# Kernel tuning notes

Measured on AMD Instinct MI355X. Metric: run time of the kernel, lower is better.

Reference implementation:

```python
import jax, jax.numpy as jnp
import numpy as np

N = 8192      # total nodes
BG = 8        # graphs in batch
NPG = 1024    # nodes per graph
DEG = 8       # in-degree per node
E = N * DEG   # edges
Q = 16        # queries per graph
D = 768       # in_dim
H = 4         # heads
F = 768       # h_feats per head
HD = H * F    # 3072


def setup_inputs() -> dict:
    key = jax.random.key(0)
    ks = jax.random.split(key, 24)
    x = jax.random.normal(ks[0], (N, D), jnp.float32)
    # block-diagonal random graph: every node has DEG incoming edges from its own graph
    edge_dst = jnp.repeat(jnp.arange(N), DEG)
    edge_src = (edge_dst // NPG) * NPG + jax.random.randint(ks[1], (E,), 0, NPG)
    query_embedding = jax.random.normal(ks[2], (BG, Q, D), jnp.float32) * 0.02
    bert_score = jax.random.uniform(ks[3], (BG, Q, NPG), jnp.float32)

    def lin(k, i, o):
        return jax.random.normal(k, (i, o), jnp.float32) * (1.0 / np.sqrt(i))

    inp = dict(x=x, edge_src=edge_src, edge_dst=edge_dst,
               query_embedding=query_embedding, bert_score=bert_score)
    inp['W1'] = lin(ks[4], D, HD)
    inp['attn_l1'] = jax.random.normal(ks[5], (H, F), jnp.float32) * 0.1
    inp['attn_r1'] = jax.random.normal(ks[6], (H, F), jnp.float32) * 0.1
    inp['b1'] = jax.random.normal(ks[7], (HD,), jnp.float32) * 0.02
    inp['gamma1'] = 1.0 + 0.1 * jax.random.normal(ks[8], (HD,), jnp.float32)
    inp['beta1'] = 0.1 * jax.random.normal(ks[9], (HD,), jnp.float32)
    inp['prelu1'] = 0.25 + 0.01 * jax.random.normal(ks[10], (HD,), jnp.float32)
    inp['W2'] = lin(ks[11], HD, HD)
    inp['attn_l2'] = jax.random.normal(ks[12], (H, F), jnp.float32) * 0.1
    inp['attn_r2'] = jax.random.normal(ks[13], (H, F), jnp.float32) * 0.1
    inp['b2'] = jax.random.normal(ks[14], (HD,), jnp.float32) * 0.02
    inp['gamma2'] = 1.0 + 0.1 * jax.random.normal(ks[15], (HD,), jnp.float32)
    inp['beta2'] = 0.1 * jax.random.normal(ks[16], (HD,), jnp.float32)
    inp['prelu2'] = 0.25 + 0.01 * jax.random.normal(ks[17], (HD,), jnp.float32)
    return inp


def _gat_layer(h, src, dst, W, al, ar, b, gamma, beta, pa):
    # DGL GATConv (eval mode, no residual): fc -> edge attention -> segment softmax -> scatter-sum
    feat = (h @ W).reshape(N, H, F)
    el = jnp.einsum('nhf,hf->nh', feat, al)            # [N,H]
    er = jnp.einsum('nhf,hf->nh', feat, ar)
    e = el[src] + er[dst]                              # [E,H]
    e = jnp.where(e > 0, e, 0.2 * e)                   # leaky_relu(0.2)
    m = jax.ops.segment_max(e, dst, num_segments=N)
    a = jnp.exp(e - m[dst])
    denom = jax.ops.segment_sum(a, dst, num_segments=N)
    alpha = a / denom[dst]                             # edge softmax over in-edges
    rst = jax.ops.segment_sum(feat[src] * alpha[:, :, None], dst, num_segments=N)
    hflat = (rst + b.reshape(1, H, F)).reshape(N, HD)
    # BatchNorm1d (training-mode batch statistics, biased var)
    mu = hflat.mean(axis=0)
    var = hflat.var(axis=0)
    hn = (hflat - mu) * jax.lax.rsqrt(var + 1e-5) * gamma + beta
    # PReLU (per-channel)
    return jnp.where(hn > 0, hn, pa * hn)


def _lambda_mrr(y_pred, y_true):
    # y_pred/y_true: [Q,K]; no padding in this pipeline (y_true = 1/rank > 0)
    order = jnp.argsort(-y_pred, axis=-1)
    yp = jnp.take_along_axis(y_pred, order, axis=-1)
    yt = jnp.take_along_axis(y_true, order, axis=-1)
    mask = (yt[:, :, None] - yt[:, None, :] > 0).astype(yp.dtype)
    sdiff = jnp.clip(yp[:, :, None] - yp[:, None, :], -50.0, 50.0)
    losses = jnp.log1p(jnp.exp(-sdiff))
    return (losses * mask).sum() / mask.sum()


def _forward(x, edge_src, edge_dst, query_embedding, bert_score,
             W1, attn_l1, attn_r1, b1, gamma1, beta1, prelu1,
             W2, attn_l2, attn_r2, b2, gamma2, beta2, prelu2):
    h1 = _gat_layer(x, edge_src, edge_dst, W1, attn_l1, attn_r1, b1, gamma1, beta1, prelu1)
    m1 = h1.reshape(N, H, F).mean(axis=1)
    h2 = _gat_layer(h1, edge_src, edge_dst, W2, attn_l2, attn_r2, b2, gamma2, beta2, prelu2)
    m2 = h2.reshape(N, H, F).mean(axis=1)
    node_rep = jnp.maximum(m1, m2)                      # JumpingKnowledge(max)

    reps = node_rep.reshape(BG, NPG, F)                 # per-graph reps
    reps_flat = node_rep                                # [N,F]
    graph_of = jnp.repeat(jnp.arange(BG), NPG)          # [N]
    rank_gt = (1.0 / jnp.arange(1, NPG + 1, dtype=jnp.float32))[None, :]  # [1,K]

    def per_graph(i, rep_i, q, bs):
        order = jnp.argsort(-bs, axis=-1)               # [Q,NPG] bert rank (desc)
        p = rep_i[order[:, 0]]                          # [Q,F] positive
        neg = rep_i[order[:, 1:]]                       # [Q,NPG-1,F] own negatives
        p_sim = jnp.sum(q * p, axis=-1, keepdims=True)  # [Q,1]
        own_sim = jnp.einsum('qf,qkf->qk', q, neg)      # [Q,NPG-1]
        all_sim = q @ reps_flat.T                       # [Q,N] for in-batch negatives
        other = (graph_of != i).astype(q.dtype)         # mask out own graph
        rank_pred = jnp.concatenate([p_sim, own_sim], axis=-1)  # first K cols of ranking_list
        mrr = _lambda_mrr(rank_pred, jnp.broadcast_to(rank_gt, rank_pred.shape))
        pe = jnp.exp(p_sim).sum(axis=-1)
        ne = jnp.exp(own_sim).sum(axis=-1) + (jnp.exp(all_sim) * other).sum(axis=-1)
        cl = jnp.mean(-jnp.log(pe / (pe + ne)))
        logp = jax.nn.log_softmax(q @ rep_i.T, axis=-1)
        ent = jnp.mean(-(jnp.exp(logp) * logp).sum(axis=-1))
        return cl, mrr, ent

    cl_g, mrr_g, ent_g = jax.vmap(per_graph)(jnp.arange(BG), reps, query_embedding, bert_score)
    return cl_g.mean(), mrr_g.mean(), ent_g.mean()


def reference(x, edge_src, edge_dst, query_embedding, bert_score,
              W1, attn_l1, attn_r1, b1, gamma1, beta1, prelu1,
              W2, attn_l2, attn_r2, b2, gamma2, beta2, prelu2):
    return _forward(x, edge_src, edge_dst, query_embedding, bert_score,
                    W1, attn_l1, attn_r1, b1, gamma1, beta1, prelu1,
                    W2, attn_l2, attn_r2, b2, gamma2, beta2, prelu2)
```

## Files before the change

kernel.cpp:

```cpp
#include <hip/hip_runtime.h>
#include <hip/hip_bf16.h>
#include <hip/hip_fp16.h>

#define NN 8192
#define DD 768
#define HH 4
#define FF 768
#define HD 3072
#define BGr 8
#define NPGr 1024
#define QQ 16
#define NQ 128
#define DEGr 8
#define MRR_TILES 36
#define WSCALE 32.0f
#define WSCALE_INV 0.03125f

typedef __attribute__((ext_vector_type(8))) short bf16x8;
typedef __attribute__((ext_vector_type(4))) float f32x4;
typedef __attribute__((ext_vector_type(4))) int i32x4;
typedef __attribute__((ext_vector_type(8))) int i32x8;

__device__ __forceinline__ unsigned short f2bf(float f) {
    union { float f; unsigned u; } v; v.f = f;
    unsigned u = v.u;
    unsigned r = (u + 0x7fffu + ((u >> 16) & 1u)) >> 16;
    return (unsigned short)r;
}
__device__ __forceinline__ float bf2f(unsigned short u) {
    union { unsigned u; float f; } v; v.u = ((unsigned)u) << 16;
    return v.f;
}
__device__ __forceinline__ unsigned char f2fp8(float x) {
    unsigned s = (__float_as_uint(x) >> 24) & 0x80;
    __half h = __float2half(fabsf(x) * 0.00390625f);
    unsigned t = (unsigned)__half_as_ushort(h);
    t += 0x3F + ((t >> 7) & 1);
    unsigned b = t >> 7;
    if (b > 0x7E) b = 0x7E;
    return (unsigned char)(s | b);
}
__device__ __forceinline__ float fp82f(unsigned u) {
    unsigned short hb = (unsigned short)(((u & 0x80) << 8) | ((u & 0x7F) << 7));
    return __half2float(__ushort_as_half(hb)) * 256.f;
}

__device__ __forceinline__ void gl_lds16(const void* g, void* l) {
    __builtin_amdgcn_global_load_lds(
        (const __attribute__((address_space(1))) unsigned int*)g,
        (__attribute__((address_space(3))) unsigned int*)l, 16, 0, 0);
}

#define PB_Z 13
#define PB_CX (PB_Z + 6144)
#define PB_CQ (PB_CX + 96)
#define PB_T1 (PB_CQ + 2304)
#define PB_T2 (PB_T1 + 9216)
__global__ __launch_bounds__(256) void prep_k(const float* __restrict__ x,
                                              unsigned char* __restrict__ xb,
                                              const float* __restrict__ qe,
                                              unsigned short* __restrict__ qeb,
                                              const float* __restrict__ W1,
                                              unsigned char* __restrict__ w1t,
                                              const float* __restrict__ W2,
                                              unsigned char* __restrict__ w2t,
                                              float* __restrict__ stats1,
                                              float* __restrict__ stats2,
                                              float* __restrict__ out) {
    __shared__ float tile[32][33];
    int blk = blockIdx.x, tid = threadIdx.x;
    if (blk < PB_Z) {
        int f = blk * 1024 + tid * 4;
        if (f < 2 * HD) *(float4*)&stats1[f] = make_float4(0.f, 0.f, 0.f, 0.f);
        else if (f < 4 * HD) *(float4*)&stats2[f - 2 * HD] = make_float4(0.f, 0.f, 0.f, 0.f);
        else if (f == 4 * HD) { out[0] = 0.f; out[1] = 0.f; out[2] = 0.f; }
    } else if (blk < PB_CX) {
        int i = (blk - PB_Z) * 256 + tid;
        float4 v = ((const float4*)x)[i];
        uchar4 o;
        o.x = f2fp8(v.x); o.y = f2fp8(v.y); o.z = f2fp8(v.z); o.w = f2fp8(v.w);
        ((uchar4*)xb)[i] = o;
    } else if (blk < PB_CQ) {
        int i = (blk - PB_CX) * 256 + tid;
        float4 v = ((const float4*)qe)[i];
        ushort4 o;
        o.x = f2bf(v.x); o.y = f2bf(v.y); o.z = f2bf(v.z); o.w = f2bf(v.w);
        ((ushort4*)qeb)[i] = o;
    } else {
        const float* in; unsigned char* outp; int K, t;
        if (blk < PB_T1) { in = W1; outp = w1t; K = DD; t = blk - PB_CQ; }
        else             { in = W2; outp = w2t; K = HD; t = blk - PB_T1; }
        int n0 = (t % 96) * 32, k0 = (t / 96) * 32;
        int tx = tid & 31, ty = tid >> 5;
        #pragma unroll
        for (int i = 0; i < 4; i++) {
            int r = ty + i * 8;
            tile[r][tx] = in[(size_t)(k0 + r) * HD + n0 + tx];
        }
        __syncthreads();
        #pragma unroll
        for (int i = 0; i < 4; i++) {
            int r = ty + i * 8;
            outp[(size_t)(n0 + r) * K + k0 + tx] = f2fp8(tile[tx][r] * WSCALE);
        }
    }
}

template <bool EPI>
__global__ __launch_bounds__(256) void gemm_fp8(const unsigned char* __restrict__ A,
                                                const unsigned char* __restrict__ BT,
                                                unsigned char* __restrict__ C,
                                                float* __restrict__ elp,
                                                float* __restrict__ erp,
                                                const float* __restrict__ al,
                                                const float* __restrict__ ar,
                                                int M, int Nc, int K, float inv_scale) {
    __shared__ __align__(16) unsigned char As[128 * 128];
    __shared__ __align__(16) unsigned char Bs[128 * 128];
    int tid = threadIdx.x;
    int m0 = blockIdx.x * 128;
    int n0 = blockIdx.y * 128;
    int w = tid >> 6, lane = tid & 63;
    int wr = w >> 1, wc = w & 1;
    int lm = lane & 15, lq = lane >> 4;

    f32x4 acc[4][4] = {};

    int srow = tid >> 3, su = tid & 7;
    const unsigned char* Ag[4];
    const unsigned char* Bg[4];
    unsigned char* AsW[4];
    unsigned char* BsW[4];
    #pragma unroll
    for (int s = 0; s < 4; s++) {
        int row = srow + 32 * s;
        int uu = su ^ (row & 7);
        Ag[s]  = A  + (size_t)(m0 + row) * K + uu * 16;
        Bg[s]  = BT + (size_t)(n0 + row) * K + uu * 16;
        AsW[s] = &As[row * 128 + su * 16];
        BsW[s] = &Bs[row * 128 + su * 16];
    }

    for (int k0 = 0; k0 < K; k0 += 128) {
        __syncthreads();
        #pragma unroll
        for (int s = 0; s < 4; s++) {
            gl_lds16(Ag[s], AsW[s]);
            gl_lds16(Bg[s], BsW[s]);
        }
        __syncthreads();

        i32x8 af[4];
        #pragma unroll
        for (int i = 0; i < 4; i++) {
            int row = wr * 64 + i * 16 + lm;
            int sw = (row & 7) << 4;
            i32x4 lo = *(const i32x4*)&As[row * 128 + ((lq * 32) ^ sw)];
            i32x4 hi = *(const i32x4*)&As[row * 128 + ((lq * 32 + 16) ^ sw)];
            i32x8 v;
            v[0] = lo[0]; v[1] = lo[1]; v[2] = lo[2]; v[3] = lo[3];
            v[4] = hi[0]; v[5] = hi[1]; v[6] = hi[2]; v[7] = hi[3];
            af[i] = v;
        }
        #pragma unroll
        for (int j = 0; j < 4; j++) {
            int row = wc * 64 + j * 16 + lm;
            int sw = (row & 7) << 4;
            i32x4 lo = *(const i32x4*)&Bs[row * 128 + ((lq * 32) ^ sw)];
            i32x4 hi = *(const i32x4*)&Bs[row * 128 + ((lq * 32 + 16) ^ sw)];
            i32x8 bv;
            bv[0] = lo[0]; bv[1] = lo[1]; bv[2] = lo[2]; bv[3] = lo[3];
            bv[4] = hi[0]; bv[5] = hi[1]; bv[6] = hi[2]; bv[7] = hi[3];
            #pragma unroll
            for (int i = 0; i < 4; i++)
                acc[i][j] = __builtin_amdgcn_mfma_scale_f32_16x16x128_f8f6f4(
                    af[i], bv, acc[i][j], 0, 0, 0, 127, 0, 127);
        }

        #pragma unroll
        for (int s = 0; s < 4; s++) { Ag[s] += 128; Bg[s] += 128; }
    }

    #pragma unroll
    for (int i = 0; i < 4; i++)
        #pragma unroll
        for (int j = 0; j < 4; j++)
            #pragma unroll
            for (int r = 0; r < 4; r++)
                acc[i][j][r] *= inv_scale;

    #pragma unroll
    for (int i = 0; i < 4; i++) {
        int row = m0 + wr * 64 + i * 16 + lq * 4;
        #pragma unroll
        for (int j = 0; j < 4; j++) {
            int col = n0 + wc * 64 + j * 16 + lm;
            #pragma unroll
            for (int r = 0; r < 4; r++)
                C[(size_t)(row + r) * Nc + col] = f2fp8(acc[i][j][r]);
        }
    }

    if (EPI) {
        int h = n0 / FF;
        int cb = (n0 % FF) >> 7;
        float alv[4], arv[4];
        #pragma unroll
        for (int j = 0; j < 4; j++) {
            int col = n0 + wc * 64 + j * 16 + lm;
            alv[j] = al[col];
            arv[j] = ar[col];
        }
        #pragma unroll
        for (int i = 0; i < 4; i++) {
            #pragma unroll
            for (int r = 0; r < 4; r++) {
                float se = acc[i][0][r] * alv[0] + acc[i][1][r] * alv[1]
                         + acc[i][2][r] * alv[2] + acc[i][3][r] * alv[3];
                float sr_ = acc[i][0][r] * arv[0] + acc[i][1][r] * arv[1]
                          + acc[i][2][r] * arv[2] + acc[i][3][r] * arv[3];
                #pragma unroll
                for (int mm = 1; mm <= 8; mm <<= 1) {
                    se  += __shfl_xor(se, mm, 64);
                    sr_ += __shfl_xor(sr_, mm, 64);
                }
                if (lm == 0) {
                    int row = m0 + wr * 64 + i * 16 + lq * 4 + r;
                    size_t slot = ((size_t)row * HH + h) * 12 + cb * 2 + wc;
                    elp[slot] = se;
                    erp[slot] = sr_;
                }
            }
        }
    }
}

__global__ __launch_bounds__(256) void gemm_bt(const unsigned short* __restrict__ A,
                                               const unsigned short* __restrict__ BT,
                                               float* __restrict__ Ct,
                                               int M, int Nc, int K) {
    __shared__ unsigned short As[128 * 64];
    __shared__ unsigned short Bs[128 * 64];
    int tid = threadIdx.x;
    int m0 = blockIdx.x * 128;
    int n0 = blockIdx.y * 128;
    int w = tid >> 6, lane = tid & 63;
    int wr = w >> 1, wc = w & 1;
    int lm = lane & 15, lq = lane >> 4;

    f32x4 acc[4][4] = {};

    int pc = tid & 7;
    const unsigned short* Ag[4];
    const unsigned short* Bg[4];
    unsigned short* AsW[4];
    unsigned short* BsW[4];
    #pragma unroll
    for (int s = 0; s < 4; s++) {
        int row = (tid >> 3) + 32 * s;
        int lc = pc ^ (row & 7);
        Ag[s]  = A  + (size_t)(m0 + row) * K + lc * 8;
        Bg[s]  = BT + (size_t)(n0 + row) * K + lc * 8;
        AsW[s] = &As[(row * 8 + pc) * 8];
        BsW[s] = &Bs[(row * 8 + pc) * 8];
    }

    for (int k0 = 0; k0 < K; k0 += 64) {
        __syncthreads();
        #pragma unroll
        for (int s = 0; s < 4; s++) {
            gl_lds16(Ag[s], AsW[s]);
            gl_lds16(Bg[s], BsW[s]);
        }
        __syncthreads();

        #pragma unroll
        for (int kk = 0; kk < 2; kk++) {
            bf16x8 af[4], bfr[4];
            #pragma unroll
            for (int i = 0; i < 4; i++) {
                int row = wr * 64 + i * 16 + lm;
                int phys = (kk * 4 + lq) ^ (row & 7);
                af[i] = *(const bf16x8*)&As[row * 64 + phys * 8];
            }
            #pragma unroll
            for (int j = 0; j < 4; j++) {
                int row = wc * 64 + j * 16 + lm;
                int phys = (kk * 4 + lq) ^ (row & 7);
                bfr[j] = *(const bf16x8*)&Bs[row * 64 + phys * 8];
            }
            #pragma unroll
            for (int i = 0; i < 4; i++)
                #pragma unroll
                for (int j = 0; j < 4; j++)
                    acc[i][j] = __builtin_amdgcn_mfma_f32_16x16x32_bf16(af[i], bfr[j], acc[i][j], 0, 0, 0);
        }

        #pragma unroll
        for (int s = 0; s < 4; s++) { Ag[s] += 64; Bg[s] += 64; }
    }

    #pragma unroll
    for (int i = 0; i < 4; i++) {
        int row = m0 + wr * 64 + i * 16 + lq * 4;
        #pragma unroll
        for (int j = 0; j < 4; j++) {
            int col = n0 + wc * 64 + j * 16 + lm;
            float4 o = make_float4(acc[i][j][0], acc[i][j][1], acc[i][j][2], acc[i][j][3]);
            *(float4*)&Ct[(size_t)col * M + row] = o;
        }
    }
}

__global__ __launch_bounds__(384) void aggregate_k(const unsigned char* __restrict__ feat,
                                                   const float* __restrict__ elp,
                                                   const float* __restrict__ erp,
                                                   const int* __restrict__ esrc,
                                                   const float* __restrict__ bias,
                                                   unsigned short* __restrict__ out) {
    int b = blockIdx.x;
    int nbase = (b & 7) * NPGr + (b >> 3) * 8;
    int t = threadIdx.x;
    __shared__ int s_src[8][DEGr];
    __shared__ float s_el[8][DEGr][HH];
    __shared__ float s_er[8][HH];
    __shared__ float s_alpha[8][DEGr][HH];
    if (t < 64) s_src[t >> 3][t & 7] = esrc[(size_t)(nbase + (t >> 3)) * DEGr + (t & 7)];
    __syncthreads();
    if (t < 256) {
        int nd = t >> 5, k = (t >> 2) & 7, h = t & 3;
        const float* pp = &elp[((size_t)s_src[nd][k] * HH + h) * 12];
        float s = 0.f;
        #pragma unroll
        for (int q = 0; q < 12; q++) s += pp[q];
        s_el[nd][k][h] = s;
    }
    if (t < 32) {
        int nd = t >> 2, h = t & 3;
        const float* pp = &erp[((size_t)(nbase + nd) * HH + h) * 12];
        float s = 0.f;
        #pragma unroll
        for (int q = 0; q < 12; q++) s += pp[q];
        s_er[nd][h] = s;
    }
    __syncthreads();
    if (t < 32) {
        int nd = t >> 2, h = t & 3;
        float e[DEGr], m = -1e30f;
        #pragma unroll
        for (int k = 0; k < DEGr; k++) {
            float v = s_el[nd][k][h] + s_er[nd][h];
            v = v > 0.f ? v : 0.2f * v;
            e[k] = v; m = fmaxf(m, v);
        }
        float d = 0.f;
        #pragma unroll
        for (int k = 0; k < DEGr; k++) { e[k] = __expf(e[k] - m); d += e[k]; }
        float inv = 1.0f / d;
        #pragma unroll
        for (int k = 0; k < DEGr; k++) s_alpha[nd][k][h] = e[k] * inv;
    }
    __syncthreads();

    int c8 = t * 8;
    int h = t / 96;
    float4 b0 = *(const float4*)&bias[c8];
    float4 b1 = *(const float4*)&bias[c8 + 4];
    float bb[8] = {b0.x, b0.y, b0.z, b0.w, b1.x, b1.y, b1.z, b1.w};
    #pragma unroll
    for (int nd = 0; nd < 8; nd++) {
        float a[8] = {bb[0], bb[1], bb[2], bb[3], bb[4], bb[5], bb[6], bb[7]};
        #pragma unroll
        for (int k = 0; k < DEGr; k++) {
            float wv = s_alpha[nd][k][h];
            unsigned long fv = *(const unsigned long*)&feat[(size_t)s_src[nd][k] * HD + c8];
            #pragma unroll
            for (int e = 0; e < 8; e++)
                a[e] += wv * fp82f((unsigned)((fv >> (8 * e)) & 0xFF));
        }
        union { unsigned short u[8]; bf16x8 v; } o;
        #pragma unroll
        for (int e = 0; e < 8; e++) o.u[e] = f2bf(a[e]);
        *(bf16x8*)&out[(size_t)(nbase + nd) * HD + c8] = o.v;
    }
}

__global__ __launch_bounds__(256) void ln_stats_k(const unsigned short* __restrict__ x,
                                                  float* __restrict__ sums) {
    int col = (blockIdx.x * 256 + threadIdx.x) * 4;
    int r0 = blockIdx.y * 128;
    float s[4] = {0.f, 0.f, 0.f, 0.f}, s2[4] = {0.f, 0.f, 0.f, 0.f};
    for (int r = r0; r < r0 + 128; r++) {
        ushort4 v = *(const ushort4*)&x[(size_t)r * HD + col];
        float f0 = bf2f(v.x), f1 = bf2f(v.y), f2 = bf2f(v.z), f3 = bf2f(v.w);
        s[0] += f0; s[1] += f1; s[2] += f2; s[3] += f3;
        s2[0] += f0 * f0; s2[1] += f1 * f1; s2[2] += f2 * f2; s2[3] += f3 * f3;
    }
    #pragma unroll
    for (int e = 0; e < 4; e++) {
        atomicAdd(&sums[col + e], s[e]);
        atomicAdd(&sums[HD + col + e], s2[e]);
    }
}

__device__ __forceinline__ void ln_vals(const unsigned short* __restrict__ x, int n, int col,
                                        const float* __restrict__ sums,
                                        const float* __restrict__ gamma,
                                        const float* __restrict__ beta,
                                        const float* __restrict__ prelu,
                                        float* val) {
    const float invN = 1.0f / (float)NN;
    ushort4 v = *(const ushort4*)&x[(size_t)n * HD + col];
    float4 sm = *(const float4*)&sums[col];
    float4 sq = *(const float4*)&sums[HD + col];
    float4 g = *(const float4*)&gamma[col];
    float4 b = *(const float4*)&beta[col];
    float4 p = *(const float4*)&prelu[col];
    float vv[4] = {bf2f(v.x), bf2f(v.y), bf2f(v.z), bf2f(v.w)};
    float ss[4] = {sm.x, sm.y, sm.z, sm.w};
    float qq[4] = {sq.x, sq.y, sq.z, sq.w};
    float gg[4] = {g.x, g.y, g.z, g.w};
    float bb[4] = {b.x, b.y, b.z, b.w};
    float pp[4] = {p.x, p.y, p.z, p.w};
    #pragma unroll
    for (int e = 0; e < 4; e++) {
        float mu = ss[e] * invN;
        float var = qq[e] * invN - mu * mu;
        float rs = rsqrtf(var + 1e-5f);
        float t = (vv[e] - mu) * rs * gg[e] + bb[e];
        val[e] = t > 0.f ? t : pp[e] * t;
    }
}

__global__ __launch_bounds__(192) void ln_norm_mean_k(const unsigned short* __restrict__ x,
                                                      const float* __restrict__ sums,
                                                      const float* __restrict__ gamma,
                                                      const float* __restrict__ beta,
                                                      const float* __restrict__ prelu,
                                                      unsigned char* __restrict__ h,
                                                      unsigned short* __restrict__ m1) {
    int n = blockIdx.x, tid = threadIdx.x;
    int c = tid * 4;
    float acc4[4] = {0.f, 0.f, 0.f, 0.f};
    #pragma unroll
    for (int hh = 0; hh < HH; hh++) {
        int col = hh * FF + c;
        float val[4];
        ln_vals(x, n, col, sums, gamma, beta, prelu, val);
        uchar4 o;
        o.x = f2fp8(val[0]); o.y = f2fp8(val[1]); o.z = f2fp8(val[2]); o.w = f2fp8(val[3]);
        *(uchar4*)&h[(size_t)n * HD + col] = o;
        #pragma unroll
        for (int e = 0; e < 4; e++) acc4[e] += val[e];
    }
    ushort4 o;
    o.x = f2bf(0.25f * acc4[0]); o.y = f2bf(0.25f * acc4[1]);
    o.z = f2bf(0.25f * acc4[2]); o.w = f2bf(0.25f * acc4[3]);
    *(ushort4*)&m1[(size_t)n * FF + c] = o;
}

__global__ __launch_bounds__(192) void ln_norm_rep_k(const unsigned short* __restrict__ x,
                                                     const float* __restrict__ sums,
                                                     const float* __restrict__ gamma,
                                                     const float* __restrict__ beta,
                                                     const float* __restrict__ prelu,
                                                     const unsigned short* __restrict__ m1,
                                                     unsigned short* __restrict__ rep) {
    int n = blockIdx.x, tid = threadIdx.x;
    int c = tid * 4;
    float acc4[4] = {0.f, 0.f, 0.f, 0.f};
    #pragma unroll
    for (int hh = 0; hh < HH; hh++) {
        int col = hh * FF + c;
        float val[4];
        ln_vals(x, n, col, sums, gamma, beta, prelu, val);
        #pragma unroll
        for (int e = 0; e < 4; e++) acc4[e] += val[e];
    }
    ushort4 m = *(const ushort4*)&m1[(size_t)n * FF + c];
    ushort4 o;
    o.x = f2bf(fmaxf(bf2f(m.x), 0.25f * acc4[0]));
    o.y = f2bf(fmaxf(bf2f(m.y), 0.25f * acc4[1]));
    o.z = f2bf(fmaxf(bf2f(m.z), 0.25f * acc4[2]));
    o.w = f2bf(fmaxf(bf2f(m.w), 0.25f * acc4[3]));
    *(ushort4*)&rep[(size_t)n * FF + c] = o;
}

__global__ __launch_bounds__(256) void loss_k(const float* __restrict__ simsQ,
                                              const float* __restrict__ bert,
                                              float* __restrict__ out) {
    __shared__ float s_ya[128];
    __shared__ float s_ba[128];
    __shared__ float red[256];
    __shared__ int redi[256];
    int tid = threadIdx.x;

    if (blockIdx.x < NQ * MRR_TILES) {
        int qq = blockIdx.x / MRR_TILES;
        int t36 = blockIdx.x % MRR_TILES;
        int I = 0, rem = t36;
        while (rem >= 8 - I) { rem -= 8 - I; I++; }
        int J = I + rem;
        int g = qq >> 4;
        const float* Y = simsQ + (size_t)qq * NN + (size_t)g * NPGr;
        const float* B = bert + (size_t)qq * NPGr;
        int a0 = I * 128, b0 = J * 128;

        if (tid < 128) s_ya[tid] = Y[a0 + tid];
        else           s_ba[tid - 128] = B[a0 + (tid - 128)];
        int bl = tid & 127;
        int bcol = b0 + bl;
        float yb = Y[bcol];
        float bbv = B[bcol];
        __syncthreads();

        const float L2E = 1.44269504f;
        int abase = (tid >> 7) * 64;
        float s = 0.f;
        if (I == J) {
            #pragma unroll 4
            for (int ai = 0; ai < 64; ai++) {
                int a = abase + ai;
                float ya = s_ya[a], ba = s_ba[a];
                float tdf = ya - yb;
                float d = (bbv > ba) ? tdf : -tdf;
                float xv = fminf(fmaxf(d, -50.f), 50.f);
                float term = __builtin_amdgcn_logf(1.0f + __builtin_amdgcn_exp2f(xv * L2E));
                s += (bl > a) ? term : 0.f;
            }
        } else {
            #pragma unroll 4
            for (int ai = 0; ai < 64; ai++) {
                int a = abase + ai;
                float ya = s_ya[a], ba = s_ba[a];
                float tdf = ya - yb;
                float d = (bbv > ba) ? tdf : -tdf;
                float xv = fminf(fmaxf(d, -50.f), 50.f);
                s += __builtin_amdgcn_logf(1.0f + __builtin_amdgcn_exp2f(xv * L2E));
            }
        }
        red[tid] = s; __syncthreads();
        for (int o = 128; o; o >>= 1) { if (tid < o) red[tid] += red[tid + o]; __syncthreads(); }
        if (tid == 0)
            atomicAdd(&out[1], red[0] * (0.69314718f / (523776.0f * (float)NQ)));
    } else {
        int qq = blockIdx.x - NQ * MRR_TILES;
        int g = qq >> 4;
        const float* S = simsQ + (size_t)qq * NN;
        const float* Sg = S + g * NPGr;
        float m = -1e30f;
        for (int n = tid; n < NN; n += 256) m = fmaxf(m, S[n]);
        red[tid] = m; __syncthreads();
        for (int o = 128; o; o >>= 1) { if (tid < o) red[tid] = fmaxf(red[tid], red[tid + o]); __syncthreads(); }
        float mAll = red[0]; __syncthreads();
        float mg = -1e30f;
        for (int j = tid; j < NPGr; j += 256) mg = fmaxf(mg, Sg[j]);
        red[tid] = mg; __syncthreads();
        for (int o = 128; o; o >>= 1) { if (tid < o) red[tid] = fmaxf(red[tid], red[tid + o]); __syncthreads(); }
        float mG = red[0]; __syncthreads();
        float z = 0.f;
        for (int n = tid; n < NN; n += 256) z += __expf(S[n] - mAll);
        red[tid] = z; __syncthreads();
        for (int o = 128; o; o >>= 1) { if (tid < o) red[tid] += red[tid + o]; __syncthreads(); }
        float Zall = red[0]; __syncthreads();
        float zg = 0.f, tg = 0.f;
        for (int j = tid; j < NPGr; j += 256) {
            float s = Sg[j];
            float e = __expf(s - mG);
            zg += e; tg += e * s;
        }
        red[tid] = zg; __syncthreads();
        for (int o = 128; o; o >>= 1) { if (tid < o) red[tid] += red[tid + o]; __syncthreads(); }
        float Zg = red[0]; __syncthreads();
        red[tid] = tg; __syncthreads();
        for (int o = 128; o; o >>= 1) { if (tid < o) red[tid] += red[tid + o]; __syncthreads(); }
        float Tg = red[0]; __syncthreads();
        float bb = -1e30f; int bi = NPGr;
        for (int j = tid; j < NPGr; j += 256) {
            float v = bert[(size_t)qq * NPGr + j];
            if (v > bb) { bb = v; bi = j; }
        }
        red[tid] = bb; redi[tid] = bi; __syncthreads();
        for (int o = 128; o; o >>= 1) {
            if (tid < o) {
                if (red[tid + o] > red[tid] || (red[tid + o] == red[tid] && redi[tid + o] < redi[tid])) {
                    red[tid] = red[tid + o]; redi[tid] = redi[tid + o];
                }
            }
            __syncthreads();
        }
        if (tid == 0) {
            float p_sim = Sg[redi[0]];
            float lse = mAll + logf(Zall);
            atomicAdd(&out[0], (lse - p_sim) * (1.0f / (float)NQ));
            float entv = (mG + logf(Zg)) - Tg / Zg;
            atomicAdd(&out[2], entv * (1.0f / (float)NQ));
        }
    }
}

extern "C" void kernel_launch(void* const* d_in, const int* in_sizes, int n_in,
                              void* d_out, int out_size, void* d_ws, size_t ws_size,
                              hipStream_t stream) {
    const float* x    = (const float*)d_in[0];
    const int* esrc   = (const int*)d_in[1];
    const float* qe   = (const float*)d_in[3];
    const float* bert = (const float*)d_in[4];
    const float* W1   = (const float*)d_in[5];
    const float* al1  = (const float*)d_in[6];
    const float* ar1  = (const float*)d_in[7];
    const float* b1   = (const float*)d_in[8];
    const float* g1   = (const float*)d_in[9];
    const float* be1  = (const float*)d_in[10];
    const float* p1   = (const float*)d_in[11];
    const float* W2   = (const float*)d_in[12];
    const float* al2  = (const float*)d_in[13];
    const float* ar2  = (const float*)d_in[14];
    const float* b2   = (const float*)d_in[15];
    const float* g2   = (const float*)d_in[16];
    const float* be2  = (const float*)d_in[17];
    const float* p2   = (const float*)d_in[18];
    float* out = (float*)d_out;
    (void)in_sizes; (void)n_in; (void)out_size; (void)ws_size;

    char* p = (char*)d_ws;
    auto alloc = [&](size_t bytes) -> void* {
        void* r = (void*)p;
        p += (bytes + 255) & ~(size_t)255;
        return r;
    };
    unsigned char*  featB = (unsigned char*)alloc((size_t)NN * HD);
    unsigned short* hflat = (unsigned short*)alloc((size_t)NN * HD * 2);
    unsigned char*  hbuf  = (unsigned char*)alloc((size_t)NN * HD);
    unsigned short* repb  = (unsigned short*)alloc((size_t)NN * FF * 2);
    unsigned char*  w1t   = (unsigned char*)alloc((size_t)HD * DD);
    unsigned char*  w2t   = (unsigned char*)alloc((size_t)HD * HD);
    unsigned short* m1    = (unsigned short*)alloc((size_t)NN * FF * 2);
    float* elp            = (float*)alloc((size_t)NN * HH * 12 * 4);
    float* erp            = (float*)alloc((size_t)NN * HH * 12 * 4);
    unsigned short* qeb   = (unsigned short*)alloc((size_t)NQ * FF * 2);
    float* simsQ          = (float*)alloc((size_t)NQ * NN * 4);
    float* stats1         = (float*)alloc((size_t)2 * HD * 4);
    float* stats2         = (float*)alloc((size_t)2 * HD * 4);
    unsigned char* xb     = (unsigned char*)repb;

    prep_k<<<PB_T2, 256, 0, stream>>>(x, xb, qe, qeb, W1, w1t, W2, w2t, stats1, stats2, out);

    gemm_fp8<true><<<dim3(NN / 128, HD / 128), 256, 0, stream>>>(
        xb, w1t, featB, elp, erp, al1, ar1, NN, HD, DD, WSCALE_INV);
    aggregate_k<<<NN / 8, 384, 0, stream>>>(featB, elp, erp, esrc, b1, hflat);
    ln_stats_k<<<dim3(HD / 1024, NN / 128), 256, 0, stream>>>(hflat, stats1);
    ln_norm_mean_k<<<NN, 192, 0, stream>>>(hflat, stats1, g1, be1, p1, hbuf, m1);

    gemm_fp8<true><<<dim3(NN / 128, HD / 128), 256, 0, stream>>>(
        hbuf, w2t, featB, elp, erp, al2, ar2, NN, HD, HD, WSCALE_INV);
    aggregate_k<<<NN / 8, 384, 0, stream>>>(featB, elp, erp, esrc, b2, hflat);
    ln_stats_k<<<dim3(HD / 1024, NN / 128), 256, 0, stream>>>(hflat, stats2);
    ln_norm_rep_k<<<NN, 192, 0, stream>>>(hflat, stats2, g2, be2, p2, m1, repb);

    gemm_bt<<<dim3(NN / 128, 1), 256, 0, stream>>>(repb, qeb, simsQ, NN, NQ, FF);

    loss_k<<<NQ * MRR_TILES + NQ, 256, 0, stream>>>(simsQ, bert, out);
}
```

Baseline: 547.4 us.

## Double-buffer LDS tiles in FP8 GEMM to overlap global loads with MFMA

The FP8 GEMM k-loop now uses two LDS buffers per operand and issues the direct global-to-LDS loads for the next k-tile before computing on the current one. Manual vmcnt waits and s_barrier replace the two __syncthreads per iteration. This is meant to hide global memory latency behind the MFMA work. In exchange LDS use doubles to 64 KB per block, which can lower occupancy, and correctness now depends on the hand-written waitcnt counts.

```diff
diff --git a/kernel.cpp b/kernel.cpp
--- a/kernel.cpp
+++ b/kernel.cpp
@@ -115,8 +115,8 @@
                                                 const float* __restrict__ al,
                                                 const float* __restrict__ ar,
                                                 int M, int Nc, int K, float inv_scale) {
-    __shared__ __align__(16) unsigned char As[128 * 128];
-    __shared__ __align__(16) unsigned char Bs[128 * 128];
+    __shared__ __align__(16) unsigned char As[2][128 * 128];
+    __shared__ __align__(16) unsigned char Bs[2][128 * 128];
     int tid = threadIdx.x;
     int m0 = blockIdx.x * 128;
     int n0 = blockIdx.y * 128;
@@ -127,36 +127,54 @@
     f32x4 acc[4][4] = {};
 
     int srow = tid >> 3, su = tid & 7;
-    const unsigned char* Ag[4];
-    const unsigned char* Bg[4];
-    unsigned char* AsW[4];
-    unsigned char* BsW[4];
+    const unsigned char* Ag0[4];
+    const unsigned char* Bg0[4];
+    unsigned char* AsW[2][4];
+    unsigned char* BsW[2][4];
     #pragma unroll
     for (int s = 0; s < 4; s++) {
         int row = srow + 32 * s;
         int uu = su ^ (row & 7);
-        Ag[s]  = A  + (size_t)(m0 + row) * K + uu * 16;
-        Bg[s]  = BT + (size_t)(n0 + row) * K + uu * 16;
-        AsW[s] = &As[row * 128 + su * 16];
-        BsW[s] = &Bs[row * 128 + su * 16];
-    }
-
-    for (int k0 = 0; k0 < K; k0 += 128) {
-        __syncthreads();
-        #pragma unroll
-        for (int s = 0; s < 4; s++) {
-            gl_lds16(Ag[s], AsW[s]);
-            gl_lds16(Bg[s], BsW[s]);
-        }
-        __syncthreads();
-
+        Ag0[s] = A  + (size_t)(m0 + row) * K + uu * 16;
+        Bg0[s] = BT + (size_t)(n0 + row) * K + uu * 16;
+        #pragma unroll
+        for (int b = 0; b < 2; b++) {
+            AsW[b][s] = &As[b][row * 128 + su * 16];
+            BsW[b][s] = &Bs[b][row * 128 + su * 16];
+        }
+    }
+
+    int NT = K >> 7;
+    #pragma unroll
+    for (int s = 0; s < 4; s++) {
+        gl_lds16(Ag0[s], AsW[0][s]);
+        gl_lds16(Bg0[s], BsW[0][s]);
+    }
+
+    for (int kt = 0; kt < NT; ++kt) {
+        int cur = kt & 1;
+        if (kt + 1 < NT) {
+            int kb = (kt + 1) << 7;
+            #pragma unroll
+            for (int s = 0; s < 4; s++) {
+                gl_lds16(Ag0[s] + kb, AsW[cur ^ 1][s]);
+                gl_lds16(Bg0[s] + kb, BsW[cur ^ 1][s]);
+            }
+            asm volatile("s_waitcnt vmcnt(8)" ::: "memory");
+        } else {
+            asm volatile("s_waitcnt vmcnt(0)" ::: "memory");
+        }
+        asm volatile("s_barrier" ::: "memory");
+
+        const unsigned char* Ab = &As[cur][0];
+        const unsigned char* Bb = &Bs[cur][0];
         i32x8 af[4];
         #pragma unroll
         for (int i = 0; i < 4; i++) {
             int row = wr * 64 + i * 16 + lm;
             int sw = (row & 7) << 4;
-            i32x4 lo = *(const i32x4*)&As[row * 128 + ((lq * 32) ^ sw)];
-            i32x4 hi = *(const i32x4*)&As[row * 128 + ((lq * 32 + 16) ^ sw)];
+            i32x4 lo = *(const i32x4*)&Ab[row * 128 + ((lq * 32) ^ sw)];
+            i32x4 hi = *(const i32x4*)&Ab[row * 128 + ((lq * 32 + 16) ^ sw)];
             i32x8 v;
             v[0] = lo[0]; v[1] = lo[1]; v[2] = lo[2]; v[3] = lo[3];
             v[4] = hi[0]; v[5] = hi[1]; v[6] = hi[2]; v[7] = hi[3];
@@ -166,8 +184,8 @@
         for (int j = 0; j < 4; j++) {
             int row = wc * 64 + j * 16 + lm;
             int sw = (row & 7) << 4;
-            i32x4 lo = *(const i32x4*)&Bs[row * 128 + ((lq * 32) ^ sw)];
-            i32x4 hi = *(const i32x4*)&Bs[row * 128 + ((lq * 32 + 16) ^ sw)];
+            i32x4 lo = *(const i32x4*)&Bb[row * 128 + ((lq * 32) ^ sw)];
+            i32x4 hi = *(const i32x4*)&Bb[row * 128 + ((lq * 32 + 16) ^ sw)];
             i32x8 bv;
             bv[0] = lo[0]; bv[1] = lo[1]; bv[2] = lo[2]; bv[3] = lo[3];
             bv[4] = hi[0]; bv[5] = hi[1]; bv[6] = hi[2]; bv[7] = hi[3];
@@ -176,9 +194,7 @@
                 acc[i][j] = __builtin_amdgcn_mfma_scale_f32_16x16x128_f8f6f4(
                     af[i], bv, acc[i][j], 0, 0, 0, 127, 0, 127);
         }
-
-        #pragma unroll
-        for (int s = 0; s < 4; s++) { Ag[s] += 128; Bg[s] += 128; }
+        asm volatile("s_barrier" ::: "memory");
     }
 
     #pragma unroll
```

New measurement: 545.4 us. Within noise of the previous version (-0.4%).
